# Performance work log

Hardware: AMD Instinct MI355X
Metric: run time of the kernel (lower is better)

Reference implementation:

```python
import jax, jax.numpy as jnp
import numpy as np

B, T, V, C, H, HS, L, DFF = 8192, 8, 65, 512, 8, 64, 6, 2048
LN_EPS = 1e-5


def _layernorm(x, g, b):
    mu = jnp.mean(x, axis=-1, keepdims=True)
    var = jnp.mean(jnp.square(x - mu), axis=-1, keepdims=True)
    return (x - mu) * jax.lax.rsqrt(var + LN_EPS) * g + b


def setup_inputs() -> dict:
    key = jax.random.key(0)
    ks = jax.random.split(key, 16)
    s = 0.02
    inp = {
        "idx": jax.random.randint(ks[0], (B, T), 0, V),
        "tok_table": jax.random.normal(ks[1], (V, C), jnp.float32) * s,
        "pos_table": jax.random.normal(ks[2], (T, C), jnp.float32) * s,
        "wq": jax.random.normal(ks[3], (L, H, C, HS), jnp.float32) * s,
        "wk": jax.random.normal(ks[4], (L, H, C, HS), jnp.float32) * s,
        "wv": jax.random.normal(ks[5], (L, H, C, HS), jnp.float32) * s,
        "proj_w": jax.random.normal(ks[6], (L, C, C), jnp.float32) * s,
        "proj_b": jnp.zeros((L, C), jnp.float32),
        "w1": jax.random.normal(ks[7], (L, C, DFF), jnp.float32) * s,
        "b1": jnp.zeros((L, DFF), jnp.float32),
        "w2": jax.random.normal(ks[8], (L, DFF, C), jnp.float32) * s,
        "b2": jnp.zeros((L, C), jnp.float32),
        "ln1_g": jnp.ones((L, C), jnp.float32),
        "ln1_b": jnp.zeros((L, C), jnp.float32),
        "ln2_g": jnp.ones((L, C), jnp.float32),
        "ln2_b": jnp.zeros((L, C), jnp.float32),
        "lm_w": jax.random.normal(ks[9], (C, V), jnp.float32) * s,
        "lm_b": jnp.zeros((V,), jnp.float32),
    }
    return inp


def reference(idx, tok_table, pos_table, wq, wk, wv, proj_w, proj_b,
              w1, b1, w2, b2, ln1_g, ln1_b, ln2_g, ln2_b, lm_w, lm_b):
    idx = idx[:, -T:]
    x = tok_table[idx] + pos_table[None, :T, :]  # [B,T,C]
    mask = jnp.tril(jnp.ones((T, T), bool))
    scale = C ** (-0.5)  # NOTE: original scales by n_embed, not head_size
    for l in range(L):
        q = jnp.einsum('btc,hcd->bhtd', x, wq[l])
        k = jnp.einsum('btc,hcd->bhtd', x, wk[l])
        v = jnp.einsum('btc,hcd->bhtd', x, wv[l])
        att = jnp.einsum('bhtd,bhsd->bhts', q, k) * scale
        att = jnp.where(mask, att, -jnp.inf)
        att = jax.nn.softmax(att, axis=-1)
        o = jnp.einsum('bhts,bhsd->bhtd', att, v)
        o = o.transpose(0, 2, 1, 3).reshape(x.shape[0], T, C)  # concat heads
        o = o @ proj_w[l] + proj_b[l]
        x = _layernorm(x + o, ln1_g[l], ln1_b[l])  # post-norm
        h = jax.nn.relu(x @ w1[l] + b1[l]) @ w2[l] + b2[l]
        x = _layernorm(x + h, ln2_g[l], ln2_b[l])
    logits = x @ lm_w + lm_b  # [B,T,V]
    return logits
```

## Files before the change

### kernel.cpp

```cpp
#include <hip/hip_runtime.h>
#include <hip/hip_bf16.h>
#include <math.h>

#define NTOK  65536
#define CDIM  512
#define NHEAD 8
#define HSZ   64
#define NLAYER 6
#define DFF   2048
#define VOCAB 65

typedef unsigned short u16;
typedef __attribute__((ext_vector_type(8))) __bf16 bf16x8;
typedef __attribute__((ext_vector_type(4))) float f32x4;
typedef __attribute__((ext_vector_type(8))) unsigned short ushort8;

__device__ __forceinline__ float b2f(u16 u) {
    union { unsigned int i; float f; } x; x.i = ((unsigned int)u) << 16; return x.f;
}
__device__ __forceinline__ u16 f2b(float f) {
    union { float f; unsigned int i; } x; x.f = f;
    unsigned int r = x.i + 0x7fffu + ((x.i >> 16) & 1u);
    return (u16)(r >> 16);
}

__device__ __forceinline__ void async16(const u16* g, u16* l) {
    __builtin_amdgcn_global_load_lds(
        (const __attribute__((address_space(1))) void*)g,
        (__attribute__((address_space(3))) void*)l, 16, 0, 0);
}

template<int EPI>
__global__ __launch_bounds__(512)
void gemm_bt(const u16* __restrict__ A, const u16* __restrict__ Bt,
             void* __restrict__ Cout, const float* __restrict__ bias,
             const u16* __restrict__ res, int K, int N, int Nout)
{
    __shared__ u16 lA[2 * 256 * 32];
    __shared__ u16 lB[2 * 128 * 32];
    const int tid  = threadIdx.x;

    const int Nx = gridDim.x;
    const int id = blockIdx.y * Nx + blockIdx.x;
    const int xcd = id & 7;
    const int j   = id >> 3;
    const int mt  = xcd + 8 * (j / Nx);
    const int nt  = j - (j / Nx) * Nx;
    const int m0  = mt * 256;
    const int n0  = nt * 128;

    const int lane = tid & 63;
    const int wv   = tid >> 6;
    const int wr   = (wv >> 1) * 64;
    const int wc   = (wv & 1) * 64;
    const int r16  = lane & 15;
    const int quad = lane >> 4;

    f32x4 acc[4][4] = {};

    const int srow = tid >> 2, skseg = (tid & 3) * 8;
    const u16* pA = A  + (size_t)(m0 + srow) * K + skseg;
    const u16* pB = Bt + (size_t)(n0 + srow) * K + skseg;
    const size_t r128K = (size_t)128 * K;
    u16* lA0 = &lA[(size_t)tid * 8];
    u16* lB0 = &lB[(size_t)tid * 8];

    for (int k0 = 0; k0 < K; k0 += 64) {
        async16(pA + k0,              lA0);
        async16(pA + r128K + k0,      lA0 + 4096);
        async16(pA + 32 + k0,         lA0 + 8192);
        async16(pA + r128K + 32 + k0, lA0 + 12288);
        async16(pB + k0,              lB0);
        async16(pB + 32 + k0,         lB0 + 4096);
        __syncthreads();

#pragma unroll
        for (int s = 0; s < 2; s++) {
            const u16* bA = &lA[s * 8192];
            const u16* bB = &lB[s * 4096];
            bf16x8 af[4], bfr[4];
#pragma unroll
            for (int i = 0; i < 4; i++)
                af[i] = *(const bf16x8*)(const void*)&bA[(wr + i * 16 + r16) * 32 + quad * 8];
#pragma unroll
            for (int jj = 0; jj < 4; jj++)
                bfr[jj] = *(const bf16x8*)(const void*)&bB[(wc + jj * 16 + r16) * 32 + quad * 8];
#pragma unroll
            for (int i = 0; i < 4; i++)
#pragma unroll
                for (int jj = 0; jj < 4; jj++)
                    acc[i][jj] = __builtin_amdgcn_mfma_f32_16x16x32_bf16(af[i], bfr[jj], acc[i][jj], 0, 0, 0);
        }
        __syncthreads();
    }

#pragma unroll
    for (int jj = 0; jj < 4; jj++) {
        const int col = n0 + wc + jj * 16 + r16;
        float bv = 0.f;
        if (EPI == 1 || EPI == 2) bv = bias[col];
        if (EPI == 3) bv = (col < Nout) ? bias[col] : 0.f;
#pragma unroll
        for (int i = 0; i < 4; i++) {
            const int row0 = m0 + wr + i * 16 + quad * 4;
#pragma unroll
            for (int r = 0; r < 4; r++) {
                float v = acc[i][jj][r] + bv;
                const size_t rr = (size_t)(row0 + r);
                if (EPI == 1) v += b2f(res[rr * N + col]);
                if (EPI == 2) v = fmaxf(v, 0.f);
                if (EPI == 3) {
                    if (col < Nout) ((float*)Cout)[rr * (size_t)Nout + col] = v;
                } else {
                    ((u16*)Cout)[rr * N + col] = f2b(v);
                }
            }
        }
    }
}

__global__ __launch_bounds__(256)
void attn_k(const u16* __restrict__ qkv, u16* __restrict__ out)
{
    __shared__ float sq[4][8][64], sk[4][8][64], sv[4][8][64], sp[4][64];
    const int w = threadIdx.x >> 6, lane = threadIdx.x & 63;
    const int unit = blockIdx.x * 4 + w;
    const int b = unit >> 3, h = unit & 7;
    const size_t base = (size_t)b * 8 * 1536 + h * 64;
#pragma unroll
    for (int t = 0; t < 8; t++) {
        sq[w][t][lane] = b2f(qkv[base + t * 1536 + lane]);
        sk[w][t][lane] = b2f(qkv[base + t * 1536 + 512 + lane]);
        sv[w][t][lane] = b2f(qkv[base + t * 1536 + 1024 + lane]);
    }
    __syncthreads();
    const int t = lane >> 3, s = lane & 7;
    float sc = -1e30f;
    if (s <= t) {
        float d = 0.f;
#pragma unroll
        for (int c = 0; c < 64; c++) d += sq[w][t][c] * sk[w][s][c];
        sc = d * 0.04419417382415922f;
    }
    float mx = sc;
#pragma unroll
    for (int m = 1; m < 8; m <<= 1) mx = fmaxf(mx, __shfl_xor(mx, m, 8));
    float e = __expf(sc - mx);
    if (s > t) e = 0.f;
    float sum = e;
#pragma unroll
    for (int m = 1; m < 8; m <<= 1) sum += __shfl_xor(sum, m, 8);
    sp[w][lane] = e / sum;
    __syncthreads();
#pragma unroll
    for (int tt = 0; tt < 8; tt++) {
        float a = 0.f;
#pragma unroll
        for (int ss = 0; ss < 8; ss++) a += sp[w][tt * 8 + ss] * sv[w][ss][lane];
        out[((size_t)b * 8 + tt) * 512 + h * 64 + lane] = f2b(a);
    }
}

__global__ __launch_bounds__(256)
void ln_k(const u16* __restrict__ y, const float* __restrict__ g,
          const float* __restrict__ be, u16* __restrict__ x)
{
    const int w = threadIdx.x >> 6, lane = threadIdx.x & 63;
    const size_t tok = (size_t)blockIdx.x * 4 + w;
    const u16* row = y + tok * 512 + lane * 8;
    ushort8 raw = *(const ushort8*)(const void*)row;
    float v[8];
#pragma unroll
    for (int i = 0; i < 8; i++) v[i] = b2f(raw[i]);
    float s = 0.f;
#pragma unroll
    for (int i = 0; i < 8; i++) s += v[i];
#pragma unroll
    for (int m = 1; m < 64; m <<= 1) s += __shfl_xor(s, m, 64);
    const float mu = s * (1.f / 512.f);
    float q = 0.f;
#pragma unroll
    for (int i = 0; i < 8; i++) { float d = v[i] - mu; q += d * d; }
#pragma unroll
    for (int m = 1; m < 64; m <<= 1) q += __shfl_xor(q, m, 64);
    const float inv = rsqrtf(q * (1.f / 512.f) + 1e-5f);
    f32x4 g0  = *(const f32x4*)(const void*)&g[lane * 8];
    f32x4 g1  = *(const f32x4*)(const void*)&g[lane * 8 + 4];
    f32x4 b0  = *(const f32x4*)(const void*)&be[lane * 8];
    f32x4 b1v = *(const f32x4*)(const void*)&be[lane * 8 + 4];
    ushort8 o;
#pragma unroll
    for (int i = 0; i < 4; i++) o[i]     = f2b((v[i] - mu) * inv * g0[i] + b0[i]);
#pragma unroll
    for (int i = 0; i < 4; i++) o[i + 4] = f2b((v[i + 4] - mu) * inv * g1[i] + b1v[i]);
    *(ushort8*)(void*)&x[tok * 512 + lane * 8] = o;
}

__global__ __launch_bounds__(256)
void embed_k(const int* __restrict__ idx, const float* __restrict__ tokt,
             const float* __restrict__ pos, u16* __restrict__ xb)
{
    const int tk = blockIdx.x;
    const int t = tk & 7;
    const int ix = idx[tk];
    const int c = threadIdx.x;
    const size_t o = (size_t)tk * 512;
    xb[o + c]       = f2b(tokt[(size_t)ix * 512 + c]       + pos[t * 512 + c]);
    xb[o + c + 256] = f2b(tokt[(size_t)ix * 512 + c + 256] + pos[t * 512 + c + 256]);
}

__global__ __launch_bounds__(256)
void conv_qkv_k(const float* __restrict__ wq, const float* __restrict__ wk,
                const float* __restrict__ wv, u16* __restrict__ out)
{
    int gid = blockIdx.x * 256 + threadIdx.x;
    int l = gid / 786432;
    int rem = gid - l * 786432;
    int j = rem >> 9, c = rem & 511;
    int sel = j >> 9;
    int jj = j & 511;
    int h = jj >> 6, d = jj & 63;
    const float* src = (sel == 0) ? wq : (sel == 1) ? wk : wv;
    out[gid] = f2b(src[(((size_t)l * 8 + h) * 512 + c) * 64 + d]);
}

__global__ __launch_bounds__(256)
void conv_t_k(const float* __restrict__ in, u16* __restrict__ out, int K, int N)
{
    int gid = blockIdx.x * 256 + threadIdx.x;
    int per = K * N;
    int l = gid / per;
    int rem = gid - l * per;
    int n = rem / K;
    int k = rem - n * K;
    out[gid] = f2b(in[(size_t)l * per + (size_t)k * N + n]);
}

__global__ __launch_bounds__(256)
void conv_lm_k(const float* __restrict__ lm_w, u16* __restrict__ out)
{
    int gid = blockIdx.x * 256 + threadIdx.x;
    int n = gid >> 9, c = gid & 511;
    out[gid] = (n < VOCAB) ? f2b(lm_w[(size_t)c * VOCAB + n]) : (u16)0;
}

extern "C" void kernel_launch(void* const* d_in, const int* in_sizes, int n_in,
                              void* d_out, int out_size, void* d_ws, size_t ws_size,
                              hipStream_t stream)
{
    const int*   idx    = (const int*)  d_in[0];
    const float* tokt   = (const float*)d_in[1];
    const float* post   = (const float*)d_in[2];
    const float* wq     = (const float*)d_in[3];
    const float* wk     = (const float*)d_in[4];
    const float* wvp    = (const float*)d_in[5];
    const float* proj_w = (const float*)d_in[6];
    const float* proj_b = (const float*)d_in[7];
    const float* w1     = (const float*)d_in[8];
    const float* b1     = (const float*)d_in[9];
    const float* w2     = (const float*)d_in[10];
    const float* b2     = (const float*)d_in[11];
    const float* ln1_g  = (const float*)d_in[12];
    const float* ln1_b  = (const float*)d_in[13];
    const float* ln2_g  = (const float*)d_in[14];
    const float* ln2_b  = (const float*)d_in[15];
    const float* lm_w   = (const float*)d_in[16];
    const float* lm_b   = (const float*)d_in[17];
    float* out = (float*)d_out;

    char* ws = (char*)d_ws;
    u16* wqkvt = (u16*)(ws + 0);
    u16* wprjt = (u16*)(ws + 9437184);
    u16* ww1t  = (u16*)(ws + 12582912);
    u16* ww2t  = (u16*)(ws + 25165824);
    u16* wlmt  = (u16*)(ws + 37748736);
    u16* xb    = (u16*)(ws + 37879808);
    char* big  = ws + 104988672;

    const size_t fixed_bytes = 104988672ull;
    int chunk = 4096;
    const int cands[4] = {65536, 32768, 16384, 8192};
    for (int i = 0; i < 4; i++) {
        if (fixed_bytes + (size_t)cands[i] * 4096ull <= ws_size) { chunk = cands[i]; break; }
    }
    const int nchunks = NTOK / chunk;
    u16* qkvc  = (u16*)big;
    u16* attnc = (u16*)(big + (size_t)chunk * 3072);
    u16* h1c   = (u16*)big;

    conv_qkv_k<<<6 * 1536 * 512 / 256, 256, 0, stream>>>(wq, wk, wvp, wqkvt);
    conv_t_k  <<<6 * 512 * 512 / 256, 256, 0, stream>>>(proj_w, wprjt, 512, 512);
    conv_t_k  <<<6 * 512 * 2048 / 256, 256, 0, stream>>>(w1, ww1t, 512, 2048);
    conv_t_k  <<<6 * 2048 * 512 / 256, 256, 0, stream>>>(w2, ww2t, 2048, 512);
    conv_lm_k <<<128 * 512 / 256, 256, 0, stream>>>(lm_w, wlmt);

    embed_k<<<NTOK, 256, 0, stream>>>(idx, tokt, post, xb);

    for (int l = 0; l < NLAYER; l++) {
        for (int c = 0; c < nchunks; c++) {
            const size_t t0 = (size_t)c * chunk;
            gemm_bt<0><<<dim3(12, chunk / 256), 512, 0, stream>>>(
                xb + t0 * 512, wqkvt + (size_t)l * 786432, qkvc,
                nullptr, nullptr, 512, 1536, 1536);
            attn_k<<<chunk / 4, 256, 0, stream>>>(qkvc, attnc);
            gemm_bt<1><<<dim3(4, chunk / 256), 512, 0, stream>>>(
                attnc, wprjt + (size_t)l * 262144, xb + t0 * 512,
                proj_b + l * 512, xb + t0 * 512, 512, 512, 512);
        }
        ln_k<<<NTOK / 4, 256, 0, stream>>>(xb, ln1_g + l * 512, ln1_b + l * 512, xb);
        for (int c = 0; c < nchunks; c++) {
            const size_t t0 = (size_t)c * chunk;
            gemm_bt<2><<<dim3(16, chunk / 256), 512, 0, stream>>>(
                xb + t0 * 512, ww1t + (size_t)l * 1048576, h1c,
                b1 + l * 2048, nullptr, 512, 2048, 2048);
            gemm_bt<1><<<dim3(4, chunk / 256), 512, 0, stream>>>(
                h1c, ww2t + (size_t)l * 1048576, xb + t0 * 512,
                b2 + l * 512, xb + t0 * 512, 2048, 512, 512);
        }
        ln_k<<<NTOK / 4, 256, 0, stream>>>(xb, ln2_g + l * 512, ln2_b + l * 512, xb);
    }

    gemm_bt<3><<<dim3(1, 256), 512, 0, stream>>>(
        xb, wlmt, out, lm_b, nullptr, 512, 128, VOCAB);
}
```

Measured before the change: 4.163 ms.

## Double-buffer GEMM K-loop, vectorize epilogue, tile weight transposes via LDS

The GEMM main loop now prefetches the next 32-wide K slice into the alternate LDS buffer while computing on the current one, which halves the per-iteration load size but allows loads to overlap MFMA work. The MFMA operands are swapped so each lane holds four consecutive output columns, letting the epilogue do vectorized bias loads, residual loads and packed bf16 stores instead of scalar ones. The weight conversion kernels are rewritten as 32x32 LDS-tiled transposes to get coalesced reads and writes. Risk: the K loop has twice as many barriers, and the epilogue layout change must match the swapped accumulator orientation.

```diff
diff --git a/kernel.cpp b/kernel.cpp
--- a/kernel.cpp
+++ b/kernel.cpp
@@ -43,9 +43,9 @@
     const int Nx = gridDim.x;
     const int id = blockIdx.y * Nx + blockIdx.x;
     const int xcd = id & 7;
-    const int j   = id >> 3;
-    const int mt  = xcd + 8 * (j / Nx);
-    const int nt  = j - (j / Nx) * Nx;
+    const int j0  = id >> 3;
+    const int mt  = xcd + 8 * (j0 / Nx);
+    const int nt  = j0 - (j0 / Nx) * Nx;
     const int m0  = mt * 256;
     const int n0  = nt * 128;
 
@@ -59,61 +59,80 @@
     f32x4 acc[4][4] = {};
 
     const int srow = tid >> 2, skseg = (tid & 3) * 8;
-    const u16* pA = A  + (size_t)(m0 + srow) * K + skseg;
-    const u16* pB = Bt + (size_t)(n0 + srow) * K + skseg;
-    const size_t r128K = (size_t)128 * K;
-    u16* lA0 = &lA[(size_t)tid * 8];
-    u16* lB0 = &lB[(size_t)tid * 8];
-
-    for (int k0 = 0; k0 < K; k0 += 64) {
-        async16(pA + k0,              lA0);
-        async16(pA + r128K + k0,      lA0 + 4096);
-        async16(pA + 32 + k0,         lA0 + 8192);
-        async16(pA + r128K + 32 + k0, lA0 + 12288);
-        async16(pB + k0,              lB0);
-        async16(pB + 32 + k0,         lB0 + 4096);
+    const u16* pA  = A  + (size_t)(m0 + srow) * K + skseg;
+    const u16* pA2 = pA + (size_t)128 * K;
+    const u16* pB  = Bt + (size_t)(n0 + srow) * K + skseg;
+    u16* lAt = &lA[(size_t)tid * 8];
+    u16* lBt = &lB[(size_t)tid * 8];
+
+    async16(pA,  lAt);
+    async16(pA2, lAt + 4096);
+    async16(pB,  lBt);
+    __syncthreads();
+
+    int s = 0;
+    for (int k0 = 0; k0 < K; k0 += 32) {
+        if (k0 + 32 < K) {
+            const int sn = (s ^ 1);
+            async16(pA  + k0 + 32, lAt + sn * 8192);
+            async16(pA2 + k0 + 32, lAt + sn * 8192 + 4096);
+            async16(pB  + k0 + 32, lBt + sn * 4096);
+        }
+        const u16* bA = &lA[s * 8192];
+        const u16* bB = &lB[s * 4096];
+        bf16x8 af[4], bfr[4];
+#pragma unroll
+        for (int i = 0; i < 4; i++)
+            af[i] = *(const bf16x8*)(const void*)&bA[(wr + i * 16 + r16) * 32 + quad * 8];
+#pragma unroll
+        for (int j = 0; j < 4; j++)
+            bfr[j] = *(const bf16x8*)(const void*)&bB[(wc + j * 16 + r16) * 32 + quad * 8];
+#pragma unroll
+        for (int j = 0; j < 4; j++)
+#pragma unroll
+            for (int i = 0; i < 4; i++)
+                acc[j][i] = __builtin_amdgcn_mfma_f32_16x16x32_bf16(bfr[j], af[i], acc[j][i], 0, 0, 0);
         __syncthreads();
-
-#pragma unroll
-        for (int s = 0; s < 2; s++) {
-            const u16* bA = &lA[s * 8192];
-            const u16* bB = &lB[s * 4096];
-            bf16x8 af[4], bfr[4];
-#pragma unroll
-            for (int i = 0; i < 4; i++)
-                af[i] = *(const bf16x8*)(const void*)&bA[(wr + i * 16 + r16) * 32 + quad * 8];
-#pragma unroll
-            for (int jj = 0; jj < 4; jj++)
-                bfr[jj] = *(const bf16x8*)(const void*)&bB[(wc + jj * 16 + r16) * 32 + quad * 8];
-#pragma unroll
-            for (int i = 0; i < 4; i++)
-#pragma unroll
-                for (int jj = 0; jj < 4; jj++)
-                    acc[i][jj] = __builtin_amdgcn_mfma_f32_16x16x32_bf16(af[i], bfr[jj], acc[i][jj], 0, 0, 0);
-        }
-        __syncthreads();
-    }
-
-#pragma unroll
-    for (int jj = 0; jj < 4; jj++) {
-        const int col = n0 + wc + jj * 16 + r16;
-        float bv = 0.f;
-        if (EPI == 1 || EPI == 2) bv = bias[col];
-        if (EPI == 3) bv = (col < Nout) ? bias[col] : 0.f;
-#pragma unroll
-        for (int i = 0; i < 4; i++) {
-            const int row0 = m0 + wr + i * 16 + quad * 4;
-#pragma unroll
-            for (int r = 0; r < 4; r++) {
-                float v = acc[i][jj][r] + bv;
-                const size_t rr = (size_t)(row0 + r);
-                if (EPI == 1) v += b2f(res[rr * N + col]);
-                if (EPI == 2) v = fmaxf(v, 0.f);
-                if (EPI == 3) {
-                    if (col < Nout) ((float*)Cout)[rr * (size_t)Nout + col] = v;
-                } else {
-                    ((u16*)Cout)[rr * N + col] = f2b(v);
+        s ^= 1;
+    }
+
+#pragma unroll
+    for (int i = 0; i < 4; i++) {
+        const int row = m0 + wr + i * 16 + r16;
+#pragma unroll
+        for (int j = 0; j < 4; j++) {
+            const int colb = n0 + wc + j * 16 + quad * 4;
+            float v[4];
+#pragma unroll
+            for (int r = 0; r < 4; r++) v[r] = acc[j][i][r];
+            if (EPI == 1 || EPI == 2) {
+                const f32x4 b4 = *(const f32x4*)(const void*)&bias[colb];
+#pragma unroll
+                for (int r = 0; r < 4; r++) v[r] += b4[r];
+            }
+            if (EPI == 1) {
+                const uint2 rv = *(const uint2*)(const void*)&res[(size_t)row * N + colb];
+                v[0] += b2f((u16)(rv.x & 0xffffu));
+                v[1] += b2f((u16)(rv.x >> 16));
+                v[2] += b2f((u16)(rv.y & 0xffffu));
+                v[3] += b2f((u16)(rv.y >> 16));
+            }
+            if (EPI == 2) {
+#pragma unroll
+                for (int r = 0; r < 4; r++) v[r] = fmaxf(v[r], 0.f);
+            }
+            if (EPI == 3) {
+#pragma unroll
+                for (int r = 0; r < 4; r++) {
+                    const int col = colb + r;
+                    if (col < Nout)
+                        ((float*)Cout)[(size_t)row * Nout + col] = v[r] + bias[col];
                 }
+            } else {
+                uint2 o;
+                o.x = (unsigned)f2b(v[0]) | ((unsigned)f2b(v[1]) << 16);
+                o.y = (unsigned)f2b(v[2]) | ((unsigned)f2b(v[3]) << 16);
+                *(uint2*)(void*)&((u16*)Cout)[(size_t)row * N + colb] = o;
             }
         }
     }
@@ -210,30 +229,43 @@
 }
 
 __global__ __launch_bounds__(256)
-void conv_qkv_k(const float* __restrict__ wq, const float* __restrict__ wk,
-                const float* __restrict__ wv, u16* __restrict__ out)
-{
-    int gid = blockIdx.x * 256 + threadIdx.x;
-    int l = gid / 786432;
-    int rem = gid - l * 786432;
-    int j = rem >> 9, c = rem & 511;
-    int sel = j >> 9;
-    int jj = j & 511;
-    int h = jj >> 6, d = jj & 63;
+void conv_t2_k(const float* __restrict__ in, u16* __restrict__ out, int K, int N)
+{
+    __shared__ float t[32][33];
+    const int tx = threadIdx.x & 31, ty4 = (threadIdx.x >> 5) * 4;
+    const int n0 = blockIdx.x * 32, k0 = blockIdx.y * 32, l = blockIdx.z;
+    const size_t per = (size_t)K * N;
+    const float* src = in + l * per;
+#pragma unroll
+    for (int r = 0; r < 4; r++)
+        t[ty4 + r][tx] = src[(size_t)(k0 + ty4 + r) * N + n0 + tx];
+    __syncthreads();
+    u16* dst = out + l * per;
+#pragma unroll
+    for (int r = 0; r < 4; r++)
+        dst[(size_t)(n0 + ty4 + r) * K + k0 + tx] = f2b(t[tx][ty4 + r]);
+}
+
+__global__ __launch_bounds__(256)
+void conv_qkv2_k(const float* __restrict__ wq, const float* __restrict__ wk,
+                 const float* __restrict__ wv, u16* __restrict__ out)
+{
+    __shared__ float t[32][33];
+    const int tx = threadIdx.x & 31, ty4 = (threadIdx.x >> 5) * 4;
+    const int c0 = blockIdx.x * 32, d0 = blockIdx.y * 32;
+    const int z = blockIdx.z;
+    const int sel = z / 48, rem = z - sel * 48;
+    const int l = rem >> 3, h = rem & 7;
     const float* src = (sel == 0) ? wq : (sel == 1) ? wk : wv;
-    out[gid] = f2b(src[(((size_t)l * 8 + h) * 512 + c) * 64 + d]);
-}
-
-__global__ __launch_bounds__(256)
-void conv_t_k(const float* __restrict__ in, u16* __restrict__ out, int K, int N)
-{
-    int gid = blockIdx.x * 256 + threadIdx.x;
-    int per = K * N;
-    int l = gid / per;
-    int rem = gid - l * per;
-    int n = rem / K;
-    int k = rem - n * K;
-    out[gid] = f2b(in[(size_t)l * per + (size_t)k * N + n]);
+    const float* sb = src + (((size_t)l * 8 + h) * 512) * 64;
+#pragma unroll
+    for (int r = 0; r < 4; r++)
+        t[ty4 + r][tx] = sb[(size_t)(c0 + ty4 + r) * 64 + d0 + tx];
+    __syncthreads();
+    u16* dst = out + (size_t)l * 786432 + (size_t)(sel * 512 + h * 64 + d0) * 512;
+#pragma unroll
+    for (int r = 0; r < 4; r++)
+        dst[(size_t)(ty4 + r) * 512 + c0 + tx] = f2b(t[tx][ty4 + r]);
 }
 
 __global__ __launch_bounds__(256)
@@ -288,11 +320,11 @@
     u16* attnc = (u16*)(big + (size_t)chunk * 3072);
     u16* h1c   = (u16*)big;
 
-    conv_qkv_k<<<6 * 1536 * 512 / 256, 256, 0, stream>>>(wq, wk, wvp, wqkvt);
-    conv_t_k  <<<6 * 512 * 512 / 256, 256, 0, stream>>>(proj_w, wprjt, 512, 512);
-    conv_t_k  <<<6 * 512 * 2048 / 256, 256, 0, stream>>>(w1, ww1t, 512, 2048);
-    conv_t_k  <<<6 * 2048 * 512 / 256, 256, 0, stream>>>(w2, ww2t, 2048, 512);
-    conv_lm_k <<<128 * 512 / 256, 256, 0, stream>>>(lm_w, wlmt);
+    conv_qkv2_k<<<dim3(16, 2, 144), 256, 0, stream>>>(wq, wk, wvp, wqkvt);
+    conv_t2_k  <<<dim3(16, 16, 6), 256, 0, stream>>>(proj_w, wprjt, 512, 512);
+    conv_t2_k  <<<dim3(64, 16, 6), 256, 0, stream>>>(w1, ww1t, 512, 2048);
+    conv_t2_k  <<<dim3(16, 64, 6), 256, 0, stream>>>(w2, ww2t, 2048, 512);
+    conv_lm_k  <<<128 * 512 / 256, 256, 0, stream>>>(lm_w, wlmt);
 
     embed_k<<<NTOK, 256, 0, stream>>>(idx, tokt, post, xb);
 
```

After: 4.468 ms. +7.3%, slower.
